# Kernel optimization log

Measured on AMD Instinct MI355X. Metric: run time of the kernel, lower is better.

Reference implementation:

```python
import jax, jax.numpy as jnp
import numpy as np

B, T, C, H = 16, 2048, 1024, 64

def setup_inputs() -> dict:
    key = jax.random.key(0)
    kx, kq, kk, kv = jax.random.split(key, 4)
    x = jax.random.normal(kx, (B, T, C), dtype=jnp.float32)
    Wq = jax.random.normal(kq, (C, H), dtype=jnp.float32) * (C ** -0.5)
    Wk = jax.random.normal(kk, (C, H), dtype=jnp.float32) * (C ** -0.5)
    Wv = jax.random.normal(kv, (C, H), dtype=jnp.float32) * (C ** -0.5)
    return {"x": x, "Wq": Wq, "Wk": Wk, "Wv": Wv}

def reference(x, Wq, Wk, Wv):
    # single causal self-attention head; dropout p=0.0 (identity)
    Tlen = x.shape[1]
    q = jnp.einsum('btc,ch->bth', x, Wq)  # [B,T,H]
    k = jnp.einsum('btc,ch->bth', x, Wk)
    v = jnp.einsum('btc,ch->bth', x, Wv)
    scale = q.shape[-1] ** -0.5
    scores = jnp.einsum('bth,bsh->bts', q, k) * scale  # [B,T,T]
    causal = jnp.tril(jnp.ones((Tlen, Tlen), dtype=bool))
    scores = jnp.where(causal, scores, -jnp.inf)
    weights = jax.nn.softmax(scores, axis=-1)
    out = jnp.einsum('bts,bsh->bth', weights, v)  # [B,T,H]
    return out
```

## Files before the change

### kernel.cpp

```cpp
#include <hip/hip_runtime.h>


typedef float  floatx4 __attribute__((ext_vector_type(4)));
typedef __bf16 bf16x8  __attribute__((ext_vector_type(8)));
typedef unsigned short ushort4v __attribute__((ext_vector_type(4)));
typedef unsigned int   uint2v   __attribute__((ext_vector_type(2)));
typedef unsigned int   uint4v   __attribute__((ext_vector_type(4)));

constexpr int Bn = 16;
constexpr int Tn = 2048;
constexpr int Cn = 1024;
constexpr int Hn = 64;
constexpr int BT = Bn * Tn;

constexpr float QSCALE = 0.125f * 1.44269504088896340736f;

__device__ __forceinline__ unsigned short f2b(float f) {
  unsigned int u = __builtin_bit_cast(unsigned int, f);
  u += 0x7fffu + ((u >> 16) & 1u);
  return (unsigned short)(u >> 16);
}

__device__ __forceinline__ unsigned int cvt_pk_bf16(float lo, float hi) {
  unsigned int r;
  asm("v_cvt_pk_bf16_f32 %0, %1, %2" : "=v"(r) : "v"(lo), "v"(hi));
  return r;
}

__global__ __launch_bounds__(256) void pack_w(const float* __restrict__ Wq,
                                              const float* __restrict__ Wk,
                                              const float* __restrict__ Wv,
                                              unsigned short* __restrict__ Wp) {
  int gid = blockIdx.x * 256 + threadIdx.x;
  int mat = gid >> 16;
  int rem = gid & 65535;
  int k   = rem >> 6;
  int col = rem & 63;
  const float* W = (mat == 0) ? Wq : (mat == 1) ? Wk : Wv;
  float v = W[rem];
  int kb = k >> 3, j = k & 7, ct = (mat << 2) | (col >> 4), c = col & 15;
  size_t idx = ((((size_t)ct * 128) + kb) * 16 + c) * 8 + j;
  Wp[idx] = f2b(v);
}

__global__ __launch_bounds__(256, 2) void proj_kernel(
    const float* __restrict__ x, const unsigned short* __restrict__ Wp,
    unsigned short* __restrict__ Q, unsigned short* __restrict__ K,
    unsigned short* __restrict__ Vt) {
  __shared__ alignas(16) unsigned short Bl[2][12 * 1024];

  const int tid  = threadIdx.x;
  const int wave = tid >> 6;
  const int lane = tid & 63;
  const int quad = lane >> 4;
  const int l16  = lane & 15;
  const int wr   = wave >> 1;
  const int wc   = wave & 1;
  const int rbase = blockIdx.x * 64;

  floatx4 acc[2][6];
#pragma unroll
  for (int a = 0; a < 2; ++a)
#pragma unroll
    for (int b = 0; b < 6; ++b) acc[a][b] = (floatx4){0.f, 0.f, 0.f, 0.f};

  const float* xp = x + (size_t)(rbase + wr * 32 + l16) * Cn + quad * 8;

  auto stageB = [&](int t, int buf) {
    const int kb0 = t << 3;
#pragma unroll
    for (int i = 0; i < 3; ++i) {
      const int ct = wave * 3 + i;
#pragma unroll
      for (int h = 0; h < 2; ++h) {
        const unsigned short* g =
            Wp + ((size_t)(ct * 128 + kb0 + h * 4 + quad) * 16 + l16) * 8;
        __builtin_amdgcn_global_load_lds(
            (const __attribute__((address_space(1))) void*)g,
            (__attribute__((address_space(3))) void*)&Bl[buf][ct * 1024 + h * 512],
            16, 0, 0);
      }
    }
  };

  auto loadX = [&](int t, floatx4 (&fa)[2][2][2]) {
    const int k0 = t * 64;
#pragma unroll
    for (int rg = 0; rg < 2; ++rg) {
      const float* bp = xp + rg * 16 * Cn + k0;
      fa[rg][0][0] = *reinterpret_cast<const floatx4*>(bp);
      fa[rg][0][1] = *reinterpret_cast<const floatx4*>(bp + 4);
      fa[rg][1][0] = *reinterpret_cast<const floatx4*>(bp + 32);
      fa[rg][1][1] = *reinterpret_cast<const floatx4*>(bp + 36);
    }
  };

  auto compute = [&](const floatx4 (&fa)[2][2][2], int buf) {
    bf16x8 af[2][2];
#pragma unroll
    for (int rg = 0; rg < 2; ++rg)
#pragma unroll
      for (int kk = 0; kk < 2; ++kk) {
        uint4v u;
        u[0] = cvt_pk_bf16(fa[rg][kk][0][0], fa[rg][kk][0][1]);
        u[1] = cvt_pk_bf16(fa[rg][kk][0][2], fa[rg][kk][0][3]);
        u[2] = cvt_pk_bf16(fa[rg][kk][1][0], fa[rg][kk][1][1]);
        u[3] = cvt_pk_bf16(fa[rg][kk][1][2], fa[rg][kk][1][3]);
        af[rg][kk] = __builtin_bit_cast(bf16x8, u);
      }
    __builtin_amdgcn_s_setprio(1);
#pragma unroll
    for (int kk = 0; kk < 2; ++kk) {
#pragma unroll
      for (int c6 = 0; c6 < 6; ++c6) {
        const int ct = wc * 6 + c6;
        bf16x8 bfr = *reinterpret_cast<const bf16x8*>(
            &Bl[buf][ct * 1024 + (kk * 4 + quad) * 128 + l16 * 8]);
        acc[0][c6] = __builtin_amdgcn_mfma_f32_16x16x32_bf16(af[0][kk], bfr, acc[0][c6], 0, 0, 0);
        acc[1][c6] = __builtin_amdgcn_mfma_f32_16x16x32_bf16(af[1][kk], bfr, acc[1][c6], 0, 0, 0);
      }
    }
    __builtin_amdgcn_s_setprio(0);
  };

  floatx4 fa0[2][2][2], fa1[2][2][2];

  loadX(0, fa0);
  stageB(0, 0);
  __syncthreads();

  for (int tt = 0; tt < 8; ++tt) {
    const int tb = tt * 2 + 1;
    loadX(tb, fa1);
    stageB(tb, 1);
    compute(fa0, 0);
    __syncthreads();
    if (tb + 1 < 16) {
      loadX(tb + 1, fa0);
      stageB(tb + 1, 0);
    }
    compute(fa1, 1);
    __syncthreads();
  }

#pragma unroll
  for (int rt = 0; rt < 2; ++rt) {
#pragma unroll
    for (int c6 = 0; c6 < 6; ++c6) {
      const int cbase  = wc * 96 + c6 * 16;
      const int rowloc = wr * 32 + rt * 16 + quad * 4;
      if (cbase < 64) {
#pragma unroll
        for (int r = 0; r < 4; ++r)
          Q[(size_t)(rbase + rowloc + r) * Hn + cbase + l16] =
              f2b(acc[rt][c6][r] * QSCALE);
      } else if (cbase < 128) {
#pragma unroll
        for (int r = 0; r < 4; ++r)
          K[(size_t)(rbase + rowloc + r) * Hn + cbase - 64 + l16] =
              f2b(acc[rt][c6][r]);
      } else {
        const int b  = rbase >> 11;
        const int t0 = (rbase & 2047) + rowloc;
        const int h  = cbase - 128 + l16;
        ushort4v v;
#pragma unroll
        for (int r = 0; r < 4; ++r) v[r] = f2b(acc[rt][c6][r]);
        *reinterpret_cast<ushort4v*>(&Vt[((size_t)b * Hn + h) * Tn + t0]) = v;
      }
    }
  }
}

__global__ __launch_bounds__(256) void flash_kernel(
    const unsigned short* __restrict__ Q, const unsigned short* __restrict__ K,
    const unsigned short* __restrict__ Vt, float* __restrict__ out) {
  __shared__ alignas(16) unsigned short P[4][16][64];
  __shared__ alignas(16) float Om[4][16][68];
  __shared__ float Ml[4][16][2];

  const int tid  = threadIdx.x;
  const int wave = tid >> 6;
  const int lane = tid & 63;
  const int quad = lane >> 4;
  const int l16  = lane & 15;

  const int xcd = blockIdx.x & 7;
  const int jb  = blockIdx.x >> 3;
  const int b   = xcd | ((jb & 1) << 3);
  const int p   = 31 - (jb >> 1);
  const int qbase = p * 64;
  const int n_tiles  = p + 1;
  const int lastTile = p;
  const size_t bbase  = (size_t)b * Tn * Hn;
  const size_t vtbase = (size_t)b * Hn * Tn;

  bf16x8 qf[4][2];
#pragma unroll
  for (int qt = 0; qt < 4; ++qt)
#pragma unroll
    for (int i = 0; i < 2; ++i)
      qf[qt][i] = *reinterpret_cast<const bf16x8*>(
          &Q[bbase + (size_t)(qbase + qt * 16 + l16) * Hn + i * 32 + quad * 8]);

  floatx4 O[4][4];
#pragma unroll
  for (int qt = 0; qt < 4; ++qt)
#pragma unroll
    for (int i = 0; i < 4; ++i) O[qt][i] = (floatx4){0.f, 0.f, 0.f, 0.f};
  float m_r[4], l_r[4];
#pragma unroll
  for (int qt = 0; qt < 4; ++qt) { m_r[qt] = -INFINITY; l_r[qt] = 0.f; }

  const int swz = (l16 & 7) << 3;

  for (int kt = wave; kt < n_tiles; kt += 4) {
    const int kvbase = kt * 64;

    bf16x8 kf[4][2];
#pragma unroll
    for (int ct = 0; ct < 4; ++ct) {
      const unsigned short* kp =
          &K[bbase + (size_t)(kvbase + ct * 16 + l16) * Hn + quad * 8];
      kf[ct][0] = *reinterpret_cast<const bf16x8*>(kp);
      kf[ct][1] = *reinterpret_cast<const bf16x8*>(kp + 32);
    }
    bf16x8 vf[4][2];
#pragma unroll
    for (int ht = 0; ht < 4; ++ht)
#pragma unroll
      for (int kk = 0; kk < 2; ++kk)
        vf[ht][kk] = *reinterpret_cast<const bf16x8*>(
            &Vt[vtbase + (size_t)(ht * 16 + l16) * Tn + kvbase + kk * 32 + quad * 8]);

#pragma unroll
    for (int half = 0; half < 2; ++half) {
      floatx4 S[2][4];
      __builtin_amdgcn_s_setprio(1);
#pragma unroll
      for (int ct = 0; ct < 4; ++ct) {
#pragma unroll
        for (int q2 = 0; q2 < 2; ++q2) {
          const int qt = half * 2 + q2;
          floatx4 s = (floatx4){0.f, 0.f, 0.f, 0.f};
          s = __builtin_amdgcn_mfma_f32_16x16x32_bf16(kf[ct][0], qf[qt][0], s, 0, 0, 0);
          s = __builtin_amdgcn_mfma_f32_16x16x32_bf16(kf[ct][1], qf[qt][1], s, 0, 0, 0);
          S[q2][ct] = s;
        }
      }
      __builtin_amdgcn_s_setprio(0);

#pragma unroll
      for (int q2 = 0; q2 < 2; ++q2) {
        const int qt = half * 2 + q2;
        const int trow = qbase + qt * 16 + l16;

        if (kt == lastTile) {
#pragma unroll
          for (int ct = 0; ct < 4; ++ct)
#pragma unroll
            for (int r = 0; r < 4; ++r)
              if (kvbase + ct * 16 + quad * 4 + r > trow) S[q2][ct][r] = -1e30f;
        }

        float mx0 = fmaxf(fmaxf(S[q2][0][0], S[q2][0][1]), fmaxf(S[q2][0][2], S[q2][0][3]));
        float mx1 = fmaxf(fmaxf(S[q2][1][0], S[q2][1][1]), fmaxf(S[q2][1][2], S[q2][1][3]));
        float mx2 = fmaxf(fmaxf(S[q2][2][0], S[q2][2][1]), fmaxf(S[q2][2][2], S[q2][2][3]));
        float mx3 = fmaxf(fmaxf(S[q2][3][0], S[q2][3][1]), fmaxf(S[q2][3][2], S[q2][3][3]));
        float mx  = fmaxf(fmaxf(mx0, mx1), fmaxf(mx2, mx3));
        mx = fmaxf(mx, __shfl_xor(mx, 16));
        mx = fmaxf(mx, __shfl_xor(mx, 32));
        if (mx > m_r[qt]) {
          float alpha = __builtin_amdgcn_exp2f(m_r[qt] - mx);
          l_r[qt] *= alpha;
#pragma unroll
          for (int ht = 0; ht < 4; ++ht)
#pragma unroll
            for (int r = 0; r < 4; ++r) O[qt][ht][r] *= alpha;
          m_r[qt] = mx;
        }
        float rs = 0.f;
#pragma unroll
        for (int ct = 0; ct < 4; ++ct)
#pragma unroll
          for (int r = 0; r < 4; ++r) {
            float pv = __builtin_amdgcn_exp2f(S[q2][ct][r] - m_r[qt]);
            S[q2][ct][r] = pv;
            rs += pv;
          }
        rs += __shfl_xor(rs, 16);
        rs += __shfl_xor(rs, 32);
        l_r[qt] += rs;

#pragma unroll
        for (int ct = 0; ct < 4; ++ct) {
          uint2v w;
          w[0] = cvt_pk_bf16(S[q2][ct][0], S[q2][ct][1]);
          w[1] = cvt_pk_bf16(S[q2][ct][2], S[q2][ct][3]);
          *reinterpret_cast<uint2v*>(&P[wave][l16][(ct * 16 + quad * 4) ^ swz]) = w;
        }
        bf16x8 pf0 = *reinterpret_cast<const bf16x8*>(&P[wave][l16][(quad * 8) ^ swz]);
        bf16x8 pf1 = *reinterpret_cast<const bf16x8*>(&P[wave][l16][(32 + quad * 8) ^ swz]);

        __builtin_amdgcn_s_setprio(1);
#pragma unroll
        for (int ht = 0; ht < 4; ++ht) {
          O[qt][ht] = __builtin_amdgcn_mfma_f32_16x16x32_bf16(vf[ht][0], pf0, O[qt][ht], 0, 0, 0);
          O[qt][ht] = __builtin_amdgcn_mfma_f32_16x16x32_bf16(vf[ht][1], pf1, O[qt][ht], 0, 0, 0);
        }
        __builtin_amdgcn_s_setprio(0);
      }
    }
  }

#pragma unroll
  for (int qt = 0; qt < 4; ++qt) {
#pragma unroll
    for (int ht = 0; ht < 4; ++ht)
#pragma unroll
      for (int r = 0; r < 4; ++r)
        Om[wave][l16][ht * 16 + quad * 4 + r] = O[qt][ht][r];
    if (quad == 0) {
      Ml[wave][l16][0] = m_r[qt];
      Ml[wave][l16][1] = l_r[qt];
    }
    __syncthreads();

    {
      const int row = tid >> 4;
      const int c4  = (tid & 15) * 4;
      float m0 = Ml[0][row][0], m1 = Ml[1][row][0];
      float m2 = Ml[2][row][0], m3 = Ml[3][row][0];
      float M = fmaxf(fmaxf(m0, m1), fmaxf(m2, m3));
      float e0 = __builtin_amdgcn_exp2f(m0 - M), e1 = __builtin_amdgcn_exp2f(m1 - M);
      float e2 = __builtin_amdgcn_exp2f(m2 - M), e3 = __builtin_amdgcn_exp2f(m3 - M);
      float L = Ml[0][row][1] * e0 + Ml[1][row][1] * e1 +
                Ml[2][row][1] * e2 + Ml[3][row][1] * e3;
      float invL = 1.0f / L;
      floatx4 o0 = *reinterpret_cast<const floatx4*>(&Om[0][row][c4]);
      floatx4 o1 = *reinterpret_cast<const floatx4*>(&Om[1][row][c4]);
      floatx4 o2 = *reinterpret_cast<const floatx4*>(&Om[2][row][c4]);
      floatx4 o3 = *reinterpret_cast<const floatx4*>(&Om[3][row][c4]);
      floatx4 res;
#pragma unroll
      for (int jj = 0; jj < 4; ++jj)
        res[jj] = (o0[jj] * e0 + o1[jj] * e1 + o2[jj] * e2 + o3[jj] * e3) * invL;
      *reinterpret_cast<floatx4*>(
          &out[bbase + (size_t)(qbase + qt * 16 + row) * Hn + c4]) = res;
    }
    __syncthreads();
  }
}

extern "C" void kernel_launch(void* const* d_in, const int* in_sizes, int n_in,
                              void* d_out, int out_size, void* d_ws, size_t ws_size,
                              hipStream_t stream) {
  const float* x  = (const float*)d_in[0];
  const float* Wq = (const float*)d_in[1];
  const float* Wk = (const float*)d_in[2];
  const float* Wv = (const float*)d_in[3];
  float* out = (float*)d_out;

  char* ws = (char*)d_ws;
  unsigned short* Q  = (unsigned short*)(ws);
  unsigned short* Kb = (unsigned short*)(ws + ((size_t)4 << 20));
  unsigned short* Vt = (unsigned short*)(ws + ((size_t)8 << 20));
  unsigned short* Wp = (unsigned short*)(ws + ((size_t)12 << 20));

  pack_w<<<dim3(768), dim3(256), 0, stream>>>(Wq, Wk, Wv, Wp);
  proj_kernel<<<dim3(BT / 64), dim3(256), 0, stream>>>(x, Wp, Q, Kb, Vt);
  flash_kernel<<<dim3(16 * 32), dim3(256), 0, stream>>>(Q, Kb, Vt, out);
}
```

Before: 246.5 us.

## Make projection waves stage private weight tiles and drop block barriers

The projection kernel is restructured to 128-thread blocks covering 32 rows, with each wave owning its own LDS copy of the 96 output columns it consumes. Because no wave reads another wave's LDS data, the __syncthreads barriers are replaced by per-wave s_waitcnt vmcnt counters and sched barriers. This removes block-level synchronisation stalls and lets waves progress independently. The cost is twice the grid size and redundant weight staging per block, which adds L2 and LDS traffic. The hand-set vmcnt values are fragile if the compiler reorders loads.

```diff
diff --git a/kernel.cpp b/kernel.cpp
--- a/kernel.cpp
+++ b/kernel.cpp
@@ -43,20 +43,18 @@
   Wp[idx] = f2b(v);
 }
 
-__global__ __launch_bounds__(256, 2) void proj_kernel(
+__global__ __launch_bounds__(128, 2) void proj_kernel(
     const float* __restrict__ x, const unsigned short* __restrict__ Wp,
     unsigned short* __restrict__ Q, unsigned short* __restrict__ K,
     unsigned short* __restrict__ Vt) {
-  __shared__ alignas(16) unsigned short Bl[2][12 * 1024];
+  __shared__ alignas(16) unsigned short Bl[2][2][6 * 1024];
 
   const int tid  = threadIdx.x;
   const int wave = tid >> 6;
   const int lane = tid & 63;
   const int quad = lane >> 4;
   const int l16  = lane & 15;
-  const int wr   = wave >> 1;
-  const int wc   = wave & 1;
-  const int rbase = blockIdx.x * 64;
+  const int rbase = blockIdx.x * 32;
 
   floatx4 acc[2][6];
 #pragma unroll
@@ -64,34 +62,35 @@
 #pragma unroll
     for (int b = 0; b < 6; ++b) acc[a][b] = (floatx4){0.f, 0.f, 0.f, 0.f};
 
-  const float* xp = x + (size_t)(rbase + wr * 32 + l16) * Cn + quad * 8;
+  const float* xp = x + (size_t)(rbase + l16) * Cn + quad * 8;
 
   auto stageB = [&](int t, int buf) {
     const int kb0 = t << 3;
 #pragma unroll
-    for (int i = 0; i < 3; ++i) {
-      const int ct = wave * 3 + i;
+    for (int c6 = 0; c6 < 6; ++c6) {
+      const int ct = wave * 6 + c6;
 #pragma unroll
       for (int h = 0; h < 2; ++h) {
         const unsigned short* g =
             Wp + ((size_t)(ct * 128 + kb0 + h * 4 + quad) * 16 + l16) * 8;
         __builtin_amdgcn_global_load_lds(
             (const __attribute__((address_space(1))) void*)g,
-            (__attribute__((address_space(3))) void*)&Bl[buf][ct * 1024 + h * 512],
+            (__attribute__((address_space(3))) void*)
+                &Bl[wave][buf][c6 * 1024 + h * 512],
             16, 0, 0);
       }
     }
   };
 
   auto loadX = [&](int t, floatx4 (&fa)[2][2][2]) {
-    const int k0 = t * 64;
+    const float* bp = xp + t * 64;
 #pragma unroll
     for (int rg = 0; rg < 2; ++rg) {
-      const float* bp = xp + rg * 16 * Cn + k0;
-      fa[rg][0][0] = *reinterpret_cast<const floatx4*>(bp);
-      fa[rg][0][1] = *reinterpret_cast<const floatx4*>(bp + 4);
-      fa[rg][1][0] = *reinterpret_cast<const floatx4*>(bp + 32);
-      fa[rg][1][1] = *reinterpret_cast<const floatx4*>(bp + 36);
+      const float* rp = bp + rg * 16 * Cn;
+      fa[rg][0][0] = *reinterpret_cast<const floatx4*>(rp);
+      fa[rg][0][1] = *reinterpret_cast<const floatx4*>(rp + 4);
+      fa[rg][1][0] = *reinterpret_cast<const floatx4*>(rp + 32);
+      fa[rg][1][1] = *reinterpret_cast<const floatx4*>(rp + 36);
     }
   };
 
@@ -113,9 +112,8 @@
     for (int kk = 0; kk < 2; ++kk) {
 #pragma unroll
       for (int c6 = 0; c6 < 6; ++c6) {
-        const int ct = wc * 6 + c6;
         bf16x8 bfr = *reinterpret_cast<const bf16x8*>(
-            &Bl[buf][ct * 1024 + (kk * 4 + quad) * 128 + l16 * 8]);
+            &Bl[wave][buf][c6 * 1024 + (kk * 4 + quad) * 128 + l16 * 8]);
         acc[0][c6] = __builtin_amdgcn_mfma_f32_16x16x32_bf16(af[0][kk], bfr, acc[0][c6], 0, 0, 0);
         acc[1][c6] = __builtin_amdgcn_mfma_f32_16x16x32_bf16(af[1][kk], bfr, acc[1][c6], 0, 0, 0);
       }
@@ -127,45 +125,48 @@
 
   loadX(0, fa0);
   stageB(0, 0);
-  __syncthreads();
 
   for (int tt = 0; tt < 8; ++tt) {
-    const int tb = tt * 2 + 1;
-    loadX(tb, fa1);
-    stageB(tb, 1);
+    const int t = tt * 2;
+    stageB(t + 1, 1);
+    loadX(t + 1, fa1);
+    asm volatile("s_waitcnt vmcnt(20)" ::: "memory");
+    __builtin_amdgcn_sched_barrier(0);
     compute(fa0, 0);
-    __syncthreads();
-    if (tb + 1 < 16) {
-      loadX(tb + 1, fa0);
-      stageB(tb + 1, 0);
-    }
+    if (t + 2 < 16) {
+      stageB(t + 2, 0);
+      loadX(t + 2, fa0);
+      asm volatile("s_waitcnt vmcnt(20)" ::: "memory");
+    } else {
+      asm volatile("s_waitcnt vmcnt(0)" ::: "memory");
+    }
+    __builtin_amdgcn_sched_barrier(0);
     compute(fa1, 1);
-    __syncthreads();
   }
 
 #pragma unroll
-  for (int rt = 0; rt < 2; ++rt) {
-#pragma unroll
-    for (int c6 = 0; c6 < 6; ++c6) {
-      const int cbase  = wc * 96 + c6 * 16;
-      const int rowloc = wr * 32 + rt * 16 + quad * 4;
+  for (int c6 = 0; c6 < 6; ++c6) {
+    const int cbase = wave * 96 + c6 * 16;
+#pragma unroll
+    for (int rg = 0; rg < 2; ++rg) {
+      const int rowloc = rg * 16 + quad * 4;
       if (cbase < 64) {
 #pragma unroll
         for (int r = 0; r < 4; ++r)
           Q[(size_t)(rbase + rowloc + r) * Hn + cbase + l16] =
-              f2b(acc[rt][c6][r] * QSCALE);
+              f2b(acc[rg][c6][r] * QSCALE);
       } else if (cbase < 128) {
 #pragma unroll
         for (int r = 0; r < 4; ++r)
           K[(size_t)(rbase + rowloc + r) * Hn + cbase - 64 + l16] =
-              f2b(acc[rt][c6][r]);
+              f2b(acc[rg][c6][r]);
       } else {
         const int b  = rbase >> 11;
         const int t0 = (rbase & 2047) + rowloc;
         const int h  = cbase - 128 + l16;
         ushort4v v;
 #pragma unroll
-        for (int r = 0; r < 4; ++r) v[r] = f2b(acc[rt][c6][r]);
+        for (int r = 0; r < 4; ++r) v[r] = f2b(acc[rg][c6][r]);
         *reinterpret_cast<ushort4v*>(&Vt[((size_t)b * Hn + h) * Tn + t0]) = v;
       }
     }
@@ -368,6 +369,6 @@
   unsigned short* Wp = (unsigned short*)(ws + ((size_t)12 << 20));
 
   pack_w<<<dim3(768), dim3(256), 0, stream>>>(Wq, Wk, Wv, Wp);
-  proj_kernel<<<dim3(BT / 64), dim3(256), 0, stream>>>(x, Wp, Q, Kb, Vt);
+  proj_kernel<<<dim3(BT / 32), dim3(128), 0, stream>>>(x, Wp, Q, Kb, Vt);
   flash_kernel<<<dim3(16 * 32), dim3(256), 0, stream>>>(Q, Kb, Vt, out);
 }
```

After: 267.1 us. +8.4%, slower.
